# Optimization experiments

Hardware: AMD Instinct MI355X
Metric: run time of the kernel (lower is better)

## Reference

```python
import jax, jax.numpy as jnp
import numpy as np

V = 200000      # num_symbols
E = 128         # embed_dim
PAD = V - 1     # padding index
KNN_K = 32
BQ, BS, NN, KT = 2048, 5, 128, 64
D = 2 * E       # d_model
STEPS = 4
H = 2 * D       # LSTMCell hidden


def setup_inputs():
    key = jax.random.key(0)
    ks = jax.random.split(key, 20)
    f = lambda k, s: jax.random.normal(k, s, dtype=jnp.float32) * 0.02
    emb = f(ks[0], (V, E)).at[PAD].set(0.0)  # padding row is zeros
    return dict(
        emb=emb,
        gcn_W=f(ks[1], (E, D)), gcn_wb=jnp.zeros((E,), jnp.float32),
        gate_W=f(ks[2], (1, D)), gate_b=jnp.zeros((1,), jnp.float32),
        se_w1=f(ks[3], (2 * D, D)), se_b1=jnp.zeros((2 * D,), jnp.float32),
        se_w2=f(ks[4], (D, 2 * D)), se_b2=jnp.zeros((D,), jnp.float32),
        ln_g=jnp.ones((D,), jnp.float32), ln_b=jnp.zeros((D,), jnp.float32),
        W_ih=f(ks[5], (4 * H, D)), W_hh=f(ks[6], (4 * H, H)),
        b_ih=jnp.zeros((4 * H,), jnp.float32), b_hh=jnp.zeros((4 * H,), jnp.float32),
        query=jax.random.randint(ks[7], (BQ, 2), 0, V),
        support=jax.random.randint(ks[8], (BS, 2), 0, V),
        q_l_conn=jax.random.randint(ks[9], (BQ, NN, 2), 0, V),
        q_l_deg=jax.random.randint(ks[10], (BQ,), 1, NN),
        q_r_conn=jax.random.randint(ks[11], (BQ, NN, 2), 0, V),
        q_r_deg=jax.random.randint(ks[12], (BQ,), 1, NN),
        s_l_conn=jax.random.randint(ks[13], (BS, NN, 2), 0, V),
        s_l_deg=jax.random.randint(ks[14], (BS,), 1, NN),
        s_r_conn=jax.random.randint(ks[15], (BS, NN, 2), 0, V),
        s_r_deg=jax.random.randint(ks[16], (BS,), 1, NN),
        knn_tab=jax.random.randint(ks[17], (V, KT), 0, V),
    )


def _cos(a, b):
    # F.cosine_similarity with eps=1e-8
    eps = 1e-8
    na = jnp.maximum(jnp.linalg.norm(a, axis=-1), eps)
    nb = jnp.maximum(jnp.linalg.norm(b, axis=-1), eps)
    return jnp.sum(a * b, axis=-1) / (na * nb)


def _neighbor_encoder(conn, eids, emb, gcn_W, gcn_wb, gate_W, gate_b, knn_tab):
    eids = jnp.where((eids < 0) | (eids >= V), PAD, eids)
    rel_e = emb[conn[..., 0]]            # [B,N,E]
    ent_e = emb[conn[..., 1]]            # [B,N,E]
    center = emb[eids][:, None, :]       # [B,1,E]
    # cosine-sim top-k neighbor selection
    sim = _cos(center, ent_e)            # [B,N]
    _, idx = jax.lax.top_k(sim, KNN_K)
    rel_k = jnp.take_along_axis(rel_e, idx[..., None], axis=1)
    ent_k = jnp.take_along_axis(ent_e, idx[..., None], axis=1)
    cat = jnp.concatenate([rel_k, ent_k], axis=-1)         # [B,k,2E]
    structural = jnp.tanh(jnp.mean(cat @ gcn_W.T + gcn_wb, axis=1))  # [B,E]
    # KNN-index branch
    kidx = knn_tab[eids]
    kidx = jnp.where((kidx < 0) | (kidx >= V), PAD, kidx)
    knn_e = emb[kidx]                    # [B,KT,E]
    sim2 = _cos(center, knn_e)
    _, idx2 = jax.lax.top_k(sim2, KNN_K)
    knn_k_e = jnp.take_along_axis(knn_e, idx2[..., None], axis=1)
    pad_rel = jnp.broadcast_to(emb[PAD], knn_k_e.shape)    # pad relation embedding
    cat2 = jnp.concatenate([pad_rel, knn_k_e], axis=-1)
    knn_mean = jnp.tanh(jnp.mean(cat2 @ gcn_W.T + gcn_wb, axis=1))
    # sigmoid gate fusing structural + knn representation
    gate_in = jnp.concatenate([structural, knn_mean], axis=-1)
    alpha = jax.nn.sigmoid(gate_in @ gate_W.T + gate_b)    # [B,1]
    return (1.0 - alpha) * structural + alpha * knn_mean


def _support_enc(x, w1, b1, w2, b2, g, b):
    h = jax.nn.relu(x @ w1.T + b1) @ w2.T + b2 + x
    mu = jnp.mean(h, axis=-1, keepdims=True)
    var = jnp.var(h, axis=-1, keepdims=True)
    return (h - mu) / jnp.sqrt(var + 1e-5) * g + b


def _query_enc(support, query, W_ih, W_hh, b_ih, b_hh):
    # GMatching LSTMCell matching network; support: [1,D], query: [B,D]
    B = query.shape[0]

    def step(carry, _):
        h_r, c = carry
        z = query @ W_ih.T + b_ih + h_r @ W_hh.T + b_hh
        i, f, g, o = jnp.split(z, 4, axis=-1)
        c2 = jax.nn.sigmoid(f) * c + jax.nn.sigmoid(i) * jnp.tanh(g)
        h2 = jax.nn.sigmoid(o) * jnp.tanh(c2)
        h = query + h2[:, :D]
        attn = jax.nn.softmax(h @ support.T, axis=1)       # [B,1]
        r = attn @ support                                  # [B,D]
        return (jnp.concatenate([h, r], axis=1), c2), h

    z0 = jnp.zeros((B, H), query.dtype)
    _, hs = jax.lax.scan(step, (z0, z0), None, length=STEPS)
    return hs[-1]


def reference(emb, gcn_W, gcn_wb, gate_W, gate_b, se_w1, se_b1, se_w2, se_b2,
              ln_g, ln_b, W_ih, W_hh, b_ih, b_hh,
              query, support, q_l_conn, q_l_deg, q_r_conn, q_r_deg,
              s_l_conn, s_l_deg, s_r_conn, s_r_deg, knn_tab):
    ne = lambda conn, eids: _neighbor_encoder(conn, eids, emb, gcn_W, gcn_wb,
                                              gate_W, gate_b, knn_tab)
    ql = ne(q_l_conn, query[:, 0])
    qr = ne(q_r_conn, query[:, 1])
    sl = ne(s_l_conn, support[:, 0])
    sr = ne(s_r_conn, support[:, 1])
    query_n = jnp.concatenate([ql, qr], axis=-1)   # [BQ,D]
    supp_n = jnp.concatenate([sl, sr], axis=-1)    # [BS,D]
    se = lambda x: _support_enc(x, se_w1, se_b1, se_w2, se_b2, ln_g, ln_b)
    support_g = jnp.mean(se(supp_n), axis=0, keepdims=True)   # [1,D]
    query_g = se(query_n)                                      # [BQ,D]
    query_f = _query_enc(support_g, query_g, W_ih, W_hh, b_ih, b_hh)
    qf = query_f / jnp.maximum(jnp.linalg.norm(query_f, axis=-1, keepdims=True), 1e-12)
    sg = support_g / jnp.maximum(jnp.linalg.norm(support_g, axis=-1, keepdims=True), 1e-12)
    return (qf @ sg.T).squeeze(-1)   # [BQ]
```

## Files before the change

### kernel.cpp

```cpp
#include <hip/hip_runtime.h>

#define Vn 200000
#define PADI 199999

typedef unsigned short ushort_t;
typedef unsigned int uint_t;
typedef __attribute__((ext_vector_type(8))) short short8;
typedef _Float16 h8v __attribute__((ext_vector_type(8)));
typedef __attribute__((ext_vector_type(4))) float float4v;

__device__ __forceinline__ float sigm(float x) { return 1.f / (1.f + expf(-x)); }
__device__ __forceinline__ float dot4(float4 a, float4 b) {
  return a.x*b.x + a.y*b.y + a.z*b.z + a.w*b.w;
}
__device__ __forceinline__ ushort_t f2h(float x) {
  return __builtin_bit_cast(ushort_t, (_Float16)x);
}

__device__ __forceinline__ float2 block_reduce2(float a, float b, float2* red) {
  #pragma unroll
  for (int off = 32; off; off >>= 1) { a += __shfl_down(a, off); b += __shfl_down(b, off); }
  __syncthreads();
  if ((threadIdx.x & 63) == 0) red[threadIdx.x >> 6] = make_float2(a, b);
  __syncthreads();
  float2 r;
  r.x = red[0].x + red[1].x + red[2].x + red[3].x;
  r.y = red[0].y + red[1].y + red[2].y + red[3].y;
  return r;
}

__global__ __launch_bounds__(256) void prep_kernel(
    const float* __restrict__ sew1, const float* __restrict__ sew2,
    const float* __restrict__ Wih, const float* __restrict__ Whh,
    const float* __restrict__ bih, const float* __restrict__ bhh,
    float* __restrict__ w1t, float* __restrict__ w2t,
    ushort_t* __restrict__ Bih, ushort_t* __restrict__ Bhh,
    float* __restrict__ bias_s) {
  int b = blockIdx.x, t = threadIdx.x;
  if (b < 512) {
    int idx = b*256 + t;
    int c = idx >> 9, r = idx & 511;
    w1t[idx] = sew1[(size_t)r*256 + c];
  } else if (b < 1024) {
    int idx = (b-512)*256 + t;
    int c = idx >> 8, r = idx & 255;
    w2t[idx] = sew2[(size_t)r*512 + c];
  } else if (b < 2816) {
    int n = b - 1024;
    Bih[(size_t)n*256 + t] = f2h(Wih[(size_t)n*256 + t]);
  } else if (b < 4608) {
    int n = b - 2816;
    Bhh[(size_t)n*256 + t] = f2h(Whh[(size_t)n*512 + t]);
  } else {
    int i = (b-4608)*256 + t;
    if (i < 1792) bias_s[i] = bih[i] + bhh[i];
  }
}

__global__ __launch_bounds__(256) void enc_kernel(
    const float* __restrict__ emb, const float* __restrict__ gcnW, const float* __restrict__ gcnb,
    const float* __restrict__ gateW, const float* __restrict__ gateb,
    const int* __restrict__ knn_tab,
    const int* __restrict__ query, const int* __restrict__ support,
    const int* __restrict__ qlc, const int* __restrict__ qrc,
    const int* __restrict__ slc, const int* __restrict__ src,
    float* __restrict__ xbuf) {
  __shared__ float center[128];
  __shared__ float simsu[192];
  __shared__ int idr[128], ide[128];
  __shared__ int kidxs[64];
  __shared__ int sel[32], sel2[32];
  __shared__ int cnt1, cnt2;
  __shared__ float catbuf[256];
  __shared__ float knnA[128], knnB[128];
  __shared__ float part1[256], part2[256];
  __shared__ float structural[128], knnm[128];
  __shared__ float2 red2[4];

  int t = threadIdx.x;
  int g = blockIdx.x;
  int eid; const int* conn; float* outp;
  if (g < 2048)      { eid = query[2*g];                 conn = qlc + (size_t)g*256;      outp = xbuf + (size_t)g*256; }
  else if (g < 4096) { int b = g-2048; eid = query[2*b+1];  conn = qrc + (size_t)b*256;   outp = xbuf + (size_t)b*256 + 128; }
  else if (g < 4101) { int b = g-4096; eid = support[2*b];  conn = slc + (size_t)b*256;   outp = xbuf + (size_t)(2048+b)*256; }
  else               { int b = g-4101; eid = support[2*b+1]; conn = src + (size_t)b*256;  outp = xbuf + (size_t)(2048+b)*256 + 128; }
  if (eid < 0 || eid >= Vn) eid = PADI;

  if (t == 0) { cnt1 = 0; cnt2 = 0; }
  if (t < 128) {
    int2 cc = ((const int2*)conn)[t];
    idr[t] = cc.x; ide[t] = cc.y;
    center[t] = emb[(size_t)eid*128 + t];
  } else if (t < 192) {
    int kk = knn_tab[(size_t)eid*64 + (t-128)];
    kidxs[t-128] = (kk < 0 || kk >= Vn) ? PADI : kk;
  }
  __syncthreads();

  int gid = t >> 4, ll = t & 15;
  float4 cen0 = *(const float4*)&center[ll*8];
  float4 cen1 = *(const float4*)&center[ll*8 + 4];
  float cn2 = dot4(cen0, cen0) + dot4(cen1, cen1);
  #pragma unroll
  for (int off = 8; off; off >>= 1) cn2 += __shfl_down(cn2, off, 16);
  cn2 = __shfl(cn2, 0, 16);
  float cn = fmaxf(sqrtf(cn2), 1e-8f);

  #pragma unroll
  for (int it = 0; it < 3; ++it) {
    int rbase = it*64 + gid*4;
    int e[4];
    #pragma unroll
    for (int rr = 0; rr < 4; ++rr) {
      int n = rbase + rr;
      e[rr] = (n < 128) ? ide[n] : kidxs[n-128];
    }
    float d[4], m[4];
    #pragma unroll
    for (int rr = 0; rr < 4; ++rr) {
      const float4* p = (const float4*)(emb + (size_t)e[rr]*128);
      float4 a = p[ll*2], bb = p[ll*2+1];
      d[rr] = dot4(a, cen0) + dot4(bb, cen1);
      m[rr] = dot4(a, a) + dot4(bb, bb);
    }
    #pragma unroll
    for (int off = 8; off; off >>= 1) {
      #pragma unroll
      for (int rr = 0; rr < 4; ++rr) {
        d[rr] += __shfl_down(d[rr], off, 16);
        m[rr] += __shfl_down(m[rr], off, 16);
      }
    }
    if (ll == 0) {
      #pragma unroll
      for (int rr = 0; rr < 4; ++rr)
        simsu[rbase+rr] = d[rr] / (cn * fmaxf(sqrtf(m[rr]), 1e-8f));
    }
  }
  __syncthreads();

  if (t < 128) {
    float my = simsu[t];
    int c = 0;
    for (int j = 0; j < 128; ++j) {
      float sj = simsu[j];
      c += (sj > my) || (sj == my && j < t);
    }
    if (c < 32) { int p = atomicAdd(&cnt1, 1); sel[p] = t; }
  } else if (t < 192) {
    int i = t - 128;
    float my = simsu[128 + i];
    int c = 0;
    for (int j = 0; j < 64; ++j) {
      float sj = simsu[128 + j];
      c += (sj > my) || (sj == my && j < i);
    }
    if (c < 32) { int p = atomicAdd(&cnt2, 1); sel2[p] = i; }
  }
  __syncthreads();

  {
    int i = t & 127;
    float a0 = 0.f, a1 = 0.f, a2 = 0.f, a3 = 0.f;
    float k0 = 0.f, k1 = 0.f;
    if (t < 128) {
      #pragma unroll 2
      for (int k = 0; k < 32; k += 4) {
        a0 += emb[(size_t)idr[sel[k+0]]*128 + i];
        a1 += emb[(size_t)idr[sel[k+1]]*128 + i];
        a2 += emb[(size_t)idr[sel[k+2]]*128 + i];
        a3 += emb[(size_t)idr[sel[k+3]]*128 + i];
      }
      catbuf[i] = (a0+a1+a2+a3) * (1.f/32.f);
      #pragma unroll 2
      for (int k = 0; k < 16; k += 2) {
        k0 += emb[(size_t)kidxs[sel2[k+0]]*128 + i];
        k1 += emb[(size_t)kidxs[sel2[k+1]]*128 + i];
      }
      knnA[i] = k0 + k1;
    } else {
      #pragma unroll 2
      for (int k = 0; k < 32; k += 4) {
        a0 += emb[(size_t)ide[sel[k+0]]*128 + i];
        a1 += emb[(size_t)ide[sel[k+1]]*128 + i];
        a2 += emb[(size_t)ide[sel[k+2]]*128 + i];
        a3 += emb[(size_t)ide[sel[k+3]]*128 + i];
      }
      catbuf[128 + i] = (a0+a1+a2+a3) * (1.f/32.f);
      #pragma unroll 2
      for (int k = 16; k < 32; k += 2) {
        k0 += emb[(size_t)kidxs[sel2[k+0]]*128 + i];
        k1 += emb[(size_t)kidxs[sel2[k+1]]*128 + i];
      }
      knnB[i] = k0 + k1;
    }
  }
  __syncthreads();

  {
    int i = t & 127, half = t >> 7;
    const float4* w1p = (const float4*)(gcnW + (size_t)i*256 + half*128);
    const float4* c1p = (const float4*)(catbuf + half*128);
    float p1 = 0.f;
    #pragma unroll 8
    for (int j = 0; j < 32; ++j) {
      float4 w = w1p[j], a = c1p[j];
      p1 += dot4(w, a);
    }
    const float4* w2p = (const float4*)(gcnW + (size_t)i*256 + 128 + half*64);
    const float4* kap = (const float4*)(knnA + half*64);
    const float4* kbp = (const float4*)(knnB + half*64);
    float p2 = 0.f;
    #pragma unroll 8
    for (int j = 0; j < 16; ++j) {
      float4 w = w2p[j], xa = kap[j], xb = kbp[j];
      float4 s = make_float4(xa.x+xb.x, xa.y+xb.y, xa.z+xb.z, xa.w+xb.w);
      p2 += dot4(w, s);
    }
    part1[t] = p1;
    part2[t] = p2 * (1.f/32.f);
  }
  __syncthreads();
  if (t < 128) {
    structural[t] = tanhf(part1[t] + part1[t+128] + gcnb[t]);
    knnm[t]       = tanhf(part2[t] + part2[t+128] + gcnb[t]);
  }
  __syncthreads();

  float gv = (t < 128) ? structural[t]*gateW[t] : knnm[t-128]*gateW[t];
  float2 rr = block_reduce2(gv, 0.f, red2);
  float alpha = sigm(rr.x + gateb[0]);
  if (t < 128) outp[t] = (1.f - alpha)*structural[t] + alpha*knnm[t];
}

__global__ __launch_bounds__(256) void qenc_kernel(
    const float* __restrict__ xin, const float* __restrict__ w1t, const float* __restrict__ b1,
    const float* __restrict__ w2t, const float* __restrict__ b2,
    const float* __restrict__ lng, const float* __restrict__ lnb,
    float* __restrict__ xout, ushort_t* __restrict__ Ah) {
  __shared__ float xs[8][256];
  __shared__ float hsm[8][512];
  __shared__ float2 red2[4];
  int t = threadIdx.x;
  int r0 = blockIdx.x * 8;
  #pragma unroll
  for (int rr = 0; rr < 8; ++rr) xs[rr][t] = xin[(size_t)(r0+rr)*256 + t];
  __syncthreads();
  #pragma unroll
  for (int uo = 0; uo < 512; uo += 256) {
    int u = uo + t;
    float bv = b1[u];
    float acc[8];
    #pragma unroll
    for (int rr = 0; rr < 8; ++rr) acc[rr] = bv;
    for (int j4 = 0; j4 < 64; ++j4) {
      float w0 = w1t[(size_t)(j4*4+0)*512 + u];
      float w1v = w1t[(size_t)(j4*4+1)*512 + u];
      float w2v = w1t[(size_t)(j4*4+2)*512 + u];
      float w3 = w1t[(size_t)(j4*4+3)*512 + u];
      #pragma unroll
      for (int rr = 0; rr < 8; ++rr) {
        float4 x = *(const float4*)&xs[rr][j4*4];
        acc[rr] += x.x*w0 + x.y*w1v + x.z*w2v + x.w*w3;
      }
    }
    #pragma unroll
    for (int rr = 0; rr < 8; ++rr) hsm[rr][u] = fmaxf(acc[rr], 0.f);
  }
  __syncthreads();
  float val[8];
  {
    float bv = b2[t];
    #pragma unroll
    for (int rr = 0; rr < 8; ++rr) val[rr] = bv + xs[rr][t];
    for (int u4 = 0; u4 < 128; ++u4) {
      float w0 = w2t[(size_t)(u4*4+0)*256 + t];
      float w1v = w2t[(size_t)(u4*4+1)*256 + t];
      float w2v = w2t[(size_t)(u4*4+2)*256 + t];
      float w3 = w2t[(size_t)(u4*4+3)*256 + t];
      #pragma unroll
      for (int rr = 0; rr < 8; ++rr) {
        float4 h4 = *(const float4*)&hsm[rr][u4*4];
        val[rr] += h4.x*w0 + h4.y*w1v + h4.z*w2v + h4.w*w3;
      }
    }
  }
  float gvv = lng[t], bv2 = lnb[t];
  for (int rr = 0; rr < 8; ++rr) {
    int r = r0 + rr;
    float2 sq = block_reduce2(val[rr], val[rr]*val[rr], red2);
    float mu  = sq.x * (1.f/256.f);
    float var = sq.y * (1.f/256.f) - mu*mu;
    float rs  = 1.f / sqrtf(var + 1e-5f);
    float ov  = (val[rr] - mu) * rs * gvv + bv2;
    xout[(size_t)r*256 + t] = ov;
    if (r < 2048) Ah[(size_t)r*256 + t] = f2h(ov);
  }
}

__global__ __launch_bounds__(256) void finalize_kernel(
    const float* __restrict__ qout, const float* __restrict__ whh,
    float* __restrict__ sg_hat, float* __restrict__ z_supp) {
  __shared__ float sg[256];
  __shared__ float2 red2[4];
  int t = threadIdx.x;
  float acc = 0.f;
  #pragma unroll
  for (int s = 0; s < 5; ++s) acc += qout[(size_t)(2048+s)*256 + t];
  float sgv = acc * 0.2f;
  sg[t] = sgv;
  float2 nn = block_reduce2(sgv*sgv, 0.f, red2);
  if (blockIdx.x == 0) sg_hat[t] = sgv / fmaxf(sqrtf(nn.x), 1e-12f);
  __syncthreads();
  int u = blockIdx.x*256 + t;
  const float4* w4 = (const float4*)(whh + (size_t)u*512 + 256);
  float a = 0.f;
  #pragma unroll 4
  for (int j4 = 0; j4 < 64; ++j4) {
    float4 wv = w4[j4];
    float4 sv = *(const float4*)&sg[j4*4];
    a += dot4(wv, sv);
  }
  z_supp[u] = a;
}

__global__ __launch_bounds__(256) void gemm_f16_kernel(
    const ushort_t* __restrict__ A, const ushort_t* __restrict__ BT,
    float* __restrict__ C, const float* __restrict__ addmat,
    const float* __restrict__ cv, int remap) {
  __shared__ ushort_t As[128*40];
  __shared__ ushort_t Bs[128*40];
  int t = threadIdx.x;
  int bx = blockIdx.x;
  if (remap) bx = (bx >> 1)*4 + (bx & 1);
  int m0 = blockIdx.y * 128, n0 = bx * 128;
  int wid = t >> 6, lane = t & 63;
  int wm = (wid >> 1) * 64, wn = (wid & 1) * 64;
  int q = lane >> 4, fr = lane & 15;
  float4v acc[4][4];
  #pragma unroll
  for (int i = 0; i < 4; ++i)
    #pragma unroll
    for (int j = 0; j < 4; ++j) acc[i][j] = (float4v)0.f;

  for (int k0 = 0; k0 < 256; k0 += 32) {
    #pragma unroll
    for (int rnd = 0; rnd < 2; ++rnd) {
      int idx = rnd*256 + t;
      int row = idx >> 2, ch = idx & 3;
      *(short8*)&As[row*40 + ch*8] = *(const short8*)(A + (size_t)(m0+row)*256 + k0 + ch*8);
      *(short8*)&Bs[row*40 + ch*8] = *(const short8*)(BT + (size_t)(n0+row)*256 + k0 + ch*8);
    }
    __syncthreads();
    short8 af[4], bg[4];
    #pragma unroll
    for (int tm = 0; tm < 4; ++tm) af[tm] = *(const short8*)&As[(wm + tm*16 + fr)*40 + q*8];
    #pragma unroll
    for (int tn = 0; tn < 4; ++tn) bg[tn] = *(const short8*)&Bs[(wn + tn*16 + fr)*40 + q*8];
    #pragma unroll
    for (int tm = 0; tm < 4; ++tm)
      #pragma unroll
      for (int tn = 0; tn < 4; ++tn)
        acc[tm][tn] = __builtin_amdgcn_mfma_f32_16x16x32_f16(
            __builtin_bit_cast(h8v, af[tm]), __builtin_bit_cast(h8v, bg[tn]),
            acc[tm][tn], 0, 0, 0);
    __syncthreads();
  }

  #pragma unroll
  for (int tm = 0; tm < 4; ++tm) {
    int gm = m0 + wm + tm*16 + q*4;
    #pragma unroll
    for (int tn = 0; tn < 4; ++tn) {
      int gn = n0 + wn + tn*16 + fr;
      float cvv = cv ? cv[gn] : 0.f;
      #pragma unroll
      for (int reg = 0; reg < 4; ++reg) {
        size_t off = (size_t)(gm + reg) * 1792 + gn;
        float x = acc[tm][tn][reg] + cvv;
        if (addmat) x += addmat[off];
        C[off] = x;
      }
    }
  }
}

__global__ __launch_bounds__(256) void gate_kernel(
    const float* __restrict__ Z, const float* __restrict__ qg,
    float* __restrict__ c, ushort_t* __restrict__ Ah, int step0) {
  int idx = blockIdx.x * 256 + threadIdx.x;
  int r = idx >> 9, j = idx & 511;
  const float* zr = Z + (size_t)r * 1792;
  float zi = zr[j], zf = zr[512 + j], zg = zr[1024 + j];
  float cold = step0 ? 0.f : c[idx];
  float c2 = sigm(zf) * cold + sigm(zi) * tanhf(zg);
  c[idx] = c2;
  if (j < 256) {
    float zo = zr[1536 + j];
    float h = qg[(size_t)r*256 + j] + sigm(zo) * tanhf(c2);
    Ah[(size_t)r*256 + j] = f2h(h);
  }
}

__global__ __launch_bounds__(256) void gatecos_kernel(
    const float* __restrict__ Z, const float* __restrict__ qg, const float* __restrict__ c,
    const float* __restrict__ sgh, float* __restrict__ out) {
  int wid = threadIdx.x >> 6, lane = threadIdx.x & 63;
  int r = blockIdx.x*4 + wid;
  const float* zr = Z + (size_t)r * 1792;
  float d = 0.f, n2 = 0.f;
  #pragma unroll
  for (int i = 0; i < 4; ++i) {
    int j = lane + i*64;
    float zi = zr[j], zf = zr[512 + j], zg = zr[1024 + j], zo = zr[1536 + j];
    float cold = c[(size_t)r*512 + j];
    float c2 = sigm(zf) * cold + sigm(zi) * tanhf(zg);
    float h = qg[(size_t)r*256 + j] + sigm(zo) * tanhf(c2);
    d += h * sgh[j];
    n2 += h * h;
  }
  #pragma unroll
  for (int off = 32; off; off >>= 1) { d += __shfl_down(d, off); n2 += __shfl_down(n2, off); }
  if (lane == 0) out[r] = d / fmaxf(sqrtf(n2), 1e-12f);
}

extern "C" void kernel_launch(void* const* d_in, const int* in_sizes, int n_in,
                              void* d_out, int out_size, void* d_ws, size_t ws_size,
                              hipStream_t stream) {
  const float* emb   = (const float*)d_in[0];
  const float* gcnW  = (const float*)d_in[1];
  const float* gcnb  = (const float*)d_in[2];
  const float* gateW = (const float*)d_in[3];
  const float* gateb = (const float*)d_in[4];
  const float* sew1  = (const float*)d_in[5];
  const float* seb1  = (const float*)d_in[6];
  const float* sew2  = (const float*)d_in[7];
  const float* seb2  = (const float*)d_in[8];
  const float* lng   = (const float*)d_in[9];
  const float* lnb   = (const float*)d_in[10];
  const float* Wih   = (const float*)d_in[11];
  const float* Whh   = (const float*)d_in[12];
  const float* bih   = (const float*)d_in[13];
  const float* bhh   = (const float*)d_in[14];
  const int* query   = (const int*)d_in[15];
  const int* support = (const int*)d_in[16];
  const int* qlc     = (const int*)d_in[17];
  const int* qrc     = (const int*)d_in[19];
  const int* slc     = (const int*)d_in[21];
  const int* src     = (const int*)d_in[23];
  const int* knn     = (const int*)d_in[25];
  float* out = (float*)d_out;

  float* w = (float*)d_ws;
  size_t o = 0;
  auto alloc = [&](size_t n) { float* p = w + o; o += (n + 15) & ~(size_t)15; return p; };
  float* xbuf      = alloc((size_t)2056*256);
  float* query_g   = alloc((size_t)2056*256);
  float* sg_hat    = alloc(256);
  float* z_supp    = alloc(2048);
  float* cbuf      = alloc((size_t)2048*512);
  float* Abuf      = alloc((size_t)2048*1792);
  float* Zbuf      = alloc((size_t)2048*1792);
  float* w1t       = alloc(256*512);
  float* w2t       = alloc(512*256);
  float* bias_s    = alloc(2048);
  ushort_t* Ah     = (ushort_t*)alloc((size_t)2048*128);
  ushort_t* Bih    = (ushort_t*)alloc((size_t)1792*128);
  ushort_t* Bhh    = (ushort_t*)alloc((size_t)1792*128);
  (void)ws_size; (void)in_sizes; (void)n_in; (void)out_size;

  prep_kernel<<<4615, 256, 0, stream>>>(sew1, sew2, Wih, Whh, bih, bhh,
                                        w1t, w2t, Bih, Bhh, bias_s);

  enc_kernel<<<4106, 256, 0, stream>>>(emb, gcnW, gcnb, gateW, gateb, knn,
                                       query, support, qlc, qrc, slc, src, xbuf);

  qenc_kernel<<<257, 256, 0, stream>>>(xbuf, w1t, seb1, w2t, seb2, lng, lnb, query_g, Ah);

  finalize_kernel<<<7, 256, 0, stream>>>(query_g, Whh, sg_hat, z_supp);

  gemm_f16_kernel<<<dim3(14,16), 256, 0, stream>>>(Ah, Bih, Abuf, nullptr, bias_s, 0);
  gate_kernel<<<4096, 256, 0, stream>>>(Abuf, query_g, cbuf, Ah, 1);
  for (int s = 1; s < 4; ++s) {
    if (s < 3) {
      gemm_f16_kernel<<<dim3(14,16), 256, 0, stream>>>(Ah, Bhh, Zbuf, Abuf, z_supp, 0);
      gate_kernel<<<4096, 256, 0, stream>>>(Zbuf, query_g, cbuf, Ah, 0);
    } else {
      gemm_f16_kernel<<<dim3(8,16), 256, 0, stream>>>(Ah, Bhh, Zbuf, Abuf, z_supp, 1);
      gatecos_kernel<<<512, 256, 0, stream>>>(Zbuf, query_g, cbuf, sg_hat, out);
    }
  }
}
```

Measured before the change: 534.3 us.

## Fuse LSTM gate into GEMM epilogue via permuted gate rows, merge prep kernels

Permutes the rows of W_ih/W_hh and the biases so that each 128-column GEMM tile holds the i/f/g/o gates for the same 32 hidden units. The LSTM gate update can then run in the GEMM epilogue through shared memory, which removes the separate gate kernels and the Z buffer round trip. Weight prep is folded into the encoder launch, and the finalize work is folded into the first GEMM launch as extra blocks. This cuts kernel launches and global traffic, at the cost of a larger padded Abuf (2048 columns instead of 1792), ping-pong A buffers, and a more complex epilogue with extra syncs.

Measured after the change: 511.1 us. 4.3% less time.

```diff
diff --git a/kernel.cpp b/kernel.cpp
--- a/kernel.cpp
+++ b/kernel.cpp
@@ -16,6 +16,10 @@
 __device__ __forceinline__ ushort_t f2h(float x) {
   return __builtin_bit_cast(ushort_t, (_Float16)x);
 }
+__device__ __forceinline__ int permrow(int n) {
+  int g = n >> 7, s = (n >> 5) & 3, q = n & 31;
+  return s*512 + g*32 + q;
+}
 
 __device__ __forceinline__ float2 block_reduce2(float a, float b, float2* red) {
   #pragma unroll
@@ -29,42 +33,20 @@
   return r;
 }
 
-__global__ __launch_bounds__(256) void prep_kernel(
-    const float* __restrict__ sew1, const float* __restrict__ sew2,
-    const float* __restrict__ Wih, const float* __restrict__ Whh,
-    const float* __restrict__ bih, const float* __restrict__ bhh,
-    float* __restrict__ w1t, float* __restrict__ w2t,
-    ushort_t* __restrict__ Bih, ushort_t* __restrict__ Bhh,
-    float* __restrict__ bias_s) {
-  int b = blockIdx.x, t = threadIdx.x;
-  if (b < 512) {
-    int idx = b*256 + t;
-    int c = idx >> 9, r = idx & 511;
-    w1t[idx] = sew1[(size_t)r*256 + c];
-  } else if (b < 1024) {
-    int idx = (b-512)*256 + t;
-    int c = idx >> 8, r = idx & 255;
-    w2t[idx] = sew2[(size_t)r*512 + c];
-  } else if (b < 2816) {
-    int n = b - 1024;
-    Bih[(size_t)n*256 + t] = f2h(Wih[(size_t)n*256 + t]);
-  } else if (b < 4608) {
-    int n = b - 2816;
-    Bhh[(size_t)n*256 + t] = f2h(Whh[(size_t)n*512 + t]);
-  } else {
-    int i = (b-4608)*256 + t;
-    if (i < 1792) bias_s[i] = bih[i] + bhh[i];
-  }
-}
-
-__global__ __launch_bounds__(256) void enc_kernel(
+__global__ __launch_bounds__(256) void encprep_kernel(
     const float* __restrict__ emb, const float* __restrict__ gcnW, const float* __restrict__ gcnb,
     const float* __restrict__ gateW, const float* __restrict__ gateb,
     const int* __restrict__ knn_tab,
     const int* __restrict__ query, const int* __restrict__ support,
     const int* __restrict__ qlc, const int* __restrict__ qrc,
     const int* __restrict__ slc, const int* __restrict__ src,
-    float* __restrict__ xbuf) {
+    float* __restrict__ xbuf,
+    const float* __restrict__ sew1, const float* __restrict__ sew2,
+    const float* __restrict__ Wih, const float* __restrict__ Whh,
+    const float* __restrict__ bih, const float* __restrict__ bhh,
+    float* __restrict__ w1t, float* __restrict__ w2t,
+    ushort_t* __restrict__ Bih, ushort_t* __restrict__ Bhh,
+    float* __restrict__ bias_p) {
   __shared__ float center[128];
   __shared__ float simsu[192];
   __shared__ int idr[128], ide[128];
@@ -79,6 +61,31 @@
 
   int t = threadIdx.x;
   int g = blockIdx.x;
+
+  if (g >= 4106) {
+    int b2 = g - 4106;
+    if (b2 < 512) {
+      int idx = b2*256 + t;
+      int c = idx >> 9, r = idx & 511;
+      w1t[idx] = sew1[(size_t)r*256 + c];
+    } else if (b2 < 1024) {
+      int idx = (b2-512)*256 + t;
+      int c = idx >> 8, r = idx & 255;
+      w2t[idx] = sew2[(size_t)r*512 + c];
+    } else if (b2 < 3072) {
+      int n = b2 - 1024;
+      Bih[(size_t)n*256 + t] = f2h(Wih[(size_t)permrow(n)*256 + t]);
+    } else if (b2 < 5120) {
+      int n = b2 - 3072;
+      Bhh[(size_t)n*256 + t] = f2h(Whh[(size_t)permrow(n)*512 + t]);
+    } else {
+      int i = (b2-5120)*256 + t;
+      int o2 = permrow(i);
+      bias_p[i] = bih[o2] + bhh[o2];
+    }
+    return;
+  }
+
   int eid; const int* conn; float* outp;
   if (g < 2048)      { eid = query[2*g];                 conn = qlc + (size_t)g*256;      outp = xbuf + (size_t)g*256; }
   else if (g < 4096) { int b = g-2048; eid = query[2*b+1];  conn = qrc + (size_t)b*256;   outp = xbuf + (size_t)b*256 + 128; }
@@ -298,42 +305,48 @@
   }
 }
 
-__global__ __launch_bounds__(256) void finalize_kernel(
-    const float* __restrict__ qout, const float* __restrict__ whh,
-    float* __restrict__ sg_hat, float* __restrict__ z_supp) {
+__global__ __launch_bounds__(256) void gemmgate_kernel(
+    const ushort_t* __restrict__ A, const ushort_t* __restrict__ BT,
+    float* __restrict__ Abuf, const float* __restrict__ cv,
+    const float* __restrict__ qg, float* __restrict__ cstate,
+    ushort_t* __restrict__ AhOut, float* __restrict__ hOut,
+    const float* __restrict__ whh_full, float* __restrict__ sg_hat,
+    float* __restrict__ z_supp, int mode) {
+  __shared__ __align__(16) char arena[64*132*4];
   __shared__ float sg[256];
   __shared__ float2 red2[4];
   int t = threadIdx.x;
-  float acc = 0.f;
-  #pragma unroll
-  for (int s = 0; s < 5; ++s) acc += qout[(size_t)(2048+s)*256 + t];
-  float sgv = acc * 0.2f;
-  sg[t] = sgv;
-  float2 nn = block_reduce2(sgv*sgv, 0.f, red2);
-  if (blockIdx.x == 0) sg_hat[t] = sgv / fmaxf(sqrtf(nn.x), 1e-12f);
-  __syncthreads();
-  int u = blockIdx.x*256 + t;
-  const float4* w4 = (const float4*)(whh + (size_t)u*512 + 256);
-  float a = 0.f;
-  #pragma unroll 4
-  for (int j4 = 0; j4 < 64; ++j4) {
-    float4 wv = w4[j4];
-    float4 sv = *(const float4*)&sg[j4*4];
-    a += dot4(wv, sv);
-  }
-  z_supp[u] = a;
-}
-
-__global__ __launch_bounds__(256) void gemm_f16_kernel(
-    const ushort_t* __restrict__ A, const ushort_t* __restrict__ BT,
-    float* __restrict__ C, const float* __restrict__ addmat,
-    const float* __restrict__ cv, int remap) {
-  __shared__ ushort_t As[128*40];
-  __shared__ ushort_t Bs[128*40];
-  int t = threadIdx.x;
-  int bx = blockIdx.x;
-  if (remap) bx = (bx >> 1)*4 + (bx & 1);
-  int m0 = blockIdx.y * 128, n0 = bx * 128;
+  int bx = blockIdx.x, by = blockIdx.y;
+
+  if (bx == 16) {
+    if (by > 8) return;
+    float acc = 0.f;
+    #pragma unroll
+    for (int s = 0; s < 5; ++s) acc += qg[(size_t)(2048+s)*256 + t];
+    sg[t] = acc * 0.2f;
+    __syncthreads();
+    if (by < 8) {
+      int up = by*256 + t;
+      const float4* w4 = (const float4*)(whh_full + (size_t)permrow(up)*512 + 256);
+      float a = 0.f;
+      #pragma unroll 4
+      for (int j4 = 0; j4 < 64; ++j4) {
+        float4 wv = w4[j4];
+        float4 sv = *(const float4*)&sg[j4*4];
+        a += dot4(wv, sv);
+      }
+      z_supp[up] = a;
+    } else {
+      float sgv = sg[t];
+      float2 nn = block_reduce2(sgv*sgv, 0.f, red2);
+      sg_hat[t] = sgv / fmaxf(sqrtf(nn.x), 1e-12f);
+    }
+    return;
+  }
+
+  ushort_t* As = (ushort_t*)arena;
+  ushort_t* Bs = As + 128*40;
+  int m0 = by * 128, n0 = bx * 128;
   int wid = t >> 6, lane = t & 63;
   int wm = (wid >> 1) * 64, wn = (wid & 1) * 64;
   int q = lane >> 4, fr = lane & 15;
@@ -373,51 +386,68 @@
     #pragma unroll
     for (int tn = 0; tn < 4; ++tn) {
       int gn = n0 + wn + tn*16 + fr;
-      float cvv = cv ? cv[gn] : 0.f;
+      float cvv = cv[gn];
       #pragma unroll
       for (int reg = 0; reg < 4; ++reg) {
-        size_t off = (size_t)(gm + reg) * 1792 + gn;
+        size_t off = (size_t)(gm + reg) * 2048 + gn;
         float x = acc[tm][tn][reg] + cvv;
-        if (addmat) x += addmat[off];
-        C[off] = x;
-      }
-    }
-  }
-}
-
-__global__ __launch_bounds__(256) void gate_kernel(
-    const float* __restrict__ Z, const float* __restrict__ qg,
-    float* __restrict__ c, ushort_t* __restrict__ Ah, int step0) {
-  int idx = blockIdx.x * 256 + threadIdx.x;
-  int r = idx >> 9, j = idx & 511;
-  const float* zr = Z + (size_t)r * 1792;
-  float zi = zr[j], zf = zr[512 + j], zg = zr[1024 + j];
-  float cold = step0 ? 0.f : c[idx];
-  float c2 = sigm(zf) * cold + sigm(zi) * tanhf(zg);
-  c[idx] = c2;
-  if (j < 256) {
-    float zo = zr[1536 + j];
-    float h = qg[(size_t)r*256 + j] + sigm(zo) * tanhf(c2);
-    Ah[(size_t)r*256 + j] = f2h(h);
-  }
-}
-
-__global__ __launch_bounds__(256) void gatecos_kernel(
-    const float* __restrict__ Z, const float* __restrict__ qg, const float* __restrict__ c,
-    const float* __restrict__ sgh, float* __restrict__ out) {
+        if (mode) x += Abuf[off];
+        else      Abuf[off] = x;
+        acc[tm][tn][reg] = x;
+      }
+    }
+  }
+
+  float* zs = (float*)arena;
+  int rl = t >> 2, j0 = (t & 3) * 8;
+  #pragma unroll
+  for (int ph = 0; ph < 2; ++ph) {
+    __syncthreads();
+    if ((wid >> 1) == ph) {
+      #pragma unroll
+      for (int tm = 0; tm < 4; ++tm)
+        #pragma unroll
+        for (int tn = 0; tn < 4; ++tn) {
+          int rloc = tm*16 + q*4;
+          int col = wn + tn*16 + fr;
+          #pragma unroll
+          for (int reg = 0; reg < 4; ++reg)
+            zs[(rloc+reg)*132 + col] = acc[tm][tn][reg];
+        }
+    }
+    __syncthreads();
+    int gm_r = m0 + ph*64 + rl;
+    #pragma unroll
+    for (int e = 0; e < 8; ++e) {
+      int jl = j0 + e;
+      float zi = zs[rl*132 + jl];
+      float zf = zs[rl*132 + 32 + jl];
+      float zg = zs[rl*132 + 64 + jl];
+      float zo = zs[rl*132 + 96 + jl];
+      int jj = bx*32 + jl;
+      float cold = mode ? cstate[(size_t)gm_r*512 + jj] : 0.f;
+      float c2 = sigm(zf) * cold + sigm(zi) * tanhf(zg);
+      if (mode != 2) cstate[(size_t)gm_r*512 + jj] = c2;
+      if (bx < 8) {
+        float h = qg[(size_t)gm_r*256 + jj] + sigm(zo) * tanhf(c2);
+        if (mode == 2) hOut[(size_t)gm_r*256 + jj] = h;
+        else           AhOut[(size_t)gm_r*256 + jj] = f2h(h);
+      }
+    }
+  }
+}
+
+__global__ __launch_bounds__(256) void cos_kernel(
+    const float* __restrict__ hbuf, const float* __restrict__ sgh, float* __restrict__ out) {
   int wid = threadIdx.x >> 6, lane = threadIdx.x & 63;
   int r = blockIdx.x*4 + wid;
-  const float* zr = Z + (size_t)r * 1792;
+  const float* hr = hbuf + (size_t)r*256;
   float d = 0.f, n2 = 0.f;
   #pragma unroll
   for (int i = 0; i < 4; ++i) {
-    int j = lane + i*64;
-    float zi = zr[j], zf = zr[512 + j], zg = zr[1024 + j], zo = zr[1536 + j];
-    float cold = c[(size_t)r*512 + j];
-    float c2 = sigm(zf) * cold + sigm(zi) * tanhf(zg);
-    float h = qg[(size_t)r*256 + j] + sigm(zo) * tanhf(c2);
-    d += h * sgh[j];
-    n2 += h * h;
+    float v = hr[lane + i*64];
+    d += v * sgh[lane + i*64];
+    n2 += v * v;
   }
   #pragma unroll
   for (int off = 32; off; off >>= 1) { d += __shfl_down(d, off); n2 += __shfl_down(n2, off); }
@@ -459,35 +489,35 @@
   float* sg_hat    = alloc(256);
   float* z_supp    = alloc(2048);
   float* cbuf      = alloc((size_t)2048*512);
-  float* Abuf      = alloc((size_t)2048*1792);
-  float* Zbuf      = alloc((size_t)2048*1792);
+  float* Abuf      = alloc((size_t)2048*2048);
+  float* hbuf      = alloc((size_t)2048*256);
   float* w1t       = alloc(256*512);
   float* w2t       = alloc(512*256);
-  float* bias_s    = alloc(2048);
-  ushort_t* Ah     = (ushort_t*)alloc((size_t)2048*128);
-  ushort_t* Bih    = (ushort_t*)alloc((size_t)1792*128);
-  ushort_t* Bhh    = (ushort_t*)alloc((size_t)1792*128);
+  float* bias_p    = alloc(2048);
+  ushort_t* AhA    = (ushort_t*)alloc((size_t)2048*128);
+  ushort_t* AhB    = (ushort_t*)alloc((size_t)2048*128);
+  ushort_t* Bih    = (ushort_t*)alloc((size_t)2048*128);
+  ushort_t* Bhh    = (ushort_t*)alloc((size_t)2048*128);
   (void)ws_size; (void)in_sizes; (void)n_in; (void)out_size;
 
-  prep_kernel<<<4615, 256, 0, stream>>>(sew1, sew2, Wih, Whh, bih, bhh,
-                                        w1t, w2t, Bih, Bhh, bias_s);
-
-  enc_kernel<<<4106, 256, 0, stream>>>(emb, gcnW, gcnb, gateW, gateb, knn,
-                                       query, support, qlc, qrc, slc, src, xbuf);
-
-  qenc_kernel<<<257, 256, 0, stream>>>(xbuf, w1t, seb1, w2t, seb2, lng, lnb, query_g, Ah);
-
-  finalize_kernel<<<7, 256, 0, stream>>>(query_g, Whh, sg_hat, z_supp);
-
-  gemm_f16_kernel<<<dim3(14,16), 256, 0, stream>>>(Ah, Bih, Abuf, nullptr, bias_s, 0);
-  gate_kernel<<<4096, 256, 0, stream>>>(Abuf, query_g, cbuf, Ah, 1);
-  for (int s = 1; s < 4; ++s) {
-    if (s < 3) {
-      gemm_f16_kernel<<<dim3(14,16), 256, 0, stream>>>(Ah, Bhh, Zbuf, Abuf, z_supp, 0);
-      gate_kernel<<<4096, 256, 0, stream>>>(Zbuf, query_g, cbuf, Ah, 0);
-    } else {
-      gemm_f16_kernel<<<dim3(8,16), 256, 0, stream>>>(Ah, Bhh, Zbuf, Abuf, z_supp, 1);
-      gatecos_kernel<<<512, 256, 0, stream>>>(Zbuf, query_g, cbuf, sg_hat, out);
-    }
-  }
-}
+  encprep_kernel<<<9234, 256, 0, stream>>>(emb, gcnW, gcnb, gateW, gateb, knn,
+                                           query, support, qlc, qrc, slc, src, xbuf,
+                                           sew1, sew2, Wih, Whh, bih, bhh,
+                                           w1t, w2t, Bih, Bhh, bias_p);
+
+  qenc_kernel<<<257, 256, 0, stream>>>(xbuf, w1t, seb1, w2t, seb2, lng, lnb, query_g, AhA);
+
+  gemmgate_kernel<<<dim3(17,16), 256, 0, stream>>>(AhA, Bih, Abuf, bias_p,
+                                                   query_g, cbuf, AhB, nullptr,
+                                                   Whh, sg_hat, z_supp, 0);
+  gemmgate_kernel<<<dim3(16,16), 256, 0, stream>>>(AhB, Bhh, Abuf, z_supp,
+                                                   query_g, cbuf, AhA, nullptr,
+                                                   Whh, sg_hat, z_supp, 1);
+  gemmgate_kernel<<<dim3(16,16), 256, 0, stream>>>(AhA, Bhh, Abuf, z_supp,
+                                                   query_g, cbuf, AhB, nullptr,
+                                                   Whh, sg_hat, z_supp, 1);
+  gemmgate_kernel<<<dim3(8,16), 256, 0, stream>>>(AhB, Bhh, Abuf, z_supp,
+                                                  query_g, cbuf, nullptr, hbuf,
+                                                  Whh, sg_hat, z_supp, 2);
+  cos_kernel<<<512, 256, 0, stream>>>(hbuf, sg_hat, out);
+}
```
